# Kernel optimization log

Measured on AMD Instinct MI355X. Metric: run time of the kernel, lower is better.

## Reference

```python
import jax, jax.numpy as jnp
import numpy as np

IN_DIM = 300
MEM_DIM = 1024
DEPTH = 14  # perfect binary tree in heap order: N = 2**DEPTH - 1 = 16383 nodes


def _init_linear(key, out_dim, in_dim):
    # torch nn.Linear default init: U(-1/sqrt(in), 1/sqrt(in)) for W and b
    s = 1.0 / np.sqrt(in_dim)
    kw, kb = jax.random.split(key)
    W = jax.random.uniform(kw, (out_dim, in_dim), jnp.float32, -s, s)
    b = jax.random.uniform(kb, (out_dim,), jnp.float32, -s, s)
    return W, b


def setup_inputs() -> dict:
    key = jax.random.key(0)
    keys = jax.random.split(key, 9)
    N = 2 ** DEPTH - 1
    inp = {"embs": jax.random.normal(keys[0], (N, IN_DIM), jnp.float32)}
    gates = [("ix", IN_DIM), ("ih", MEM_DIM), ("fx", IN_DIM), ("fh", MEM_DIM),
             ("ox", IN_DIM), ("oh", MEM_DIM), ("ux", IN_DIM), ("uh", MEM_DIM)]
    for k, (name, d) in zip(keys[1:], gates):
        W, b = _init_linear(k, MEM_DIM, d)
        inp["W" + name] = W
        inp["b" + name] = b
    inp["depth"] = DEPTH
    return inp


def _lin(x, W, b):
    return x @ W.T + b


def reference(embs, Wix, bix, Wih, bih, Wfx, bfx, Wfh, bfh,
              Wox, box, Woh, boh, Wux, bux, Wuh, buh, depth):
    # Child-Sum TreeLSTM on a perfect binary tree (heap order), processed
    # bottom-up, batching all nodes of a level into single GEMMs.
    h = c = None
    for lvl in range(depth - 1, -1, -1):
        n = 2 ** lvl
        x = embs[n - 1:2 * n - 1]  # [n, in_dim], nodes of this level
        if h is None:
            # leaves: original code feeds a single zero child -> h_sum = 0
            # and f * child_c = 0 regardless of f
            hsum = jnp.zeros((n, MEM_DIM), embs.dtype)
            fc = jnp.zeros((n, MEM_DIM), embs.dtype)
        else:
            hc = h.reshape(n, 2, MEM_DIM)  # children hidden states
            cc = c.reshape(n, 2, MEM_DIM)  # children cell states
            hsum = hc.sum(axis=1)
            # per-child forget gate: sigmoid(fh(h_k) + fx(x))
            f = jax.nn.sigmoid(jnp.einsum('nkd,md->nkm', hc, Wfh) + bfh
                               + _lin(x, Wfx, bfx)[:, None, :])
            fc = (f * cc).sum(axis=1)
        i = jax.nn.sigmoid(_lin(x, Wix, bix) + _lin(hsum, Wih, bih))
        o = jax.nn.sigmoid(_lin(x, Wox, box) + _lin(hsum, Woh, boh))
        u = jnp.tanh(_lin(x, Wux, bux) + _lin(hsum, Wuh, buh))
        c = i * u + fc
        h = o * jnp.tanh(c)
    return jnp.stack([c[0], h[0]])  # root state (c, h): [2, MEM_DIM]
```

## Files before the change

kernel.cpp:

```cpp
#include <hip/hip_runtime.h>
#include <hip/hip_bf16.h>

#define IN_DIM 300
#define XDIM   320
#define MEM    1024
#define NTREE  16383

typedef _Float16 half8 __attribute__((ext_vector_type(8)));
typedef float    f32x4 __attribute__((ext_vector_type(4)));

__device__ __forceinline__ float sigf(float x) { return 1.0f / (1.0f + __expf(-x)); }
__device__ __forceinline__ float tanhfast(float x) { return 2.0f / (1.0f + __expf(-2.0f * x)) - 1.0f; }

#define GLOAD_LDS16(g, l) \
    __builtin_amdgcn_global_load_lds((const __attribute__((address_space(1))) void*)(g), \
                                     (__attribute__((address_space(3))) void*)(l), 16, 0, 0)

__global__ void pack_kernel(
    const float* __restrict__ embs,
    const float* __restrict__ Wix, const float* __restrict__ bix,
    const float* __restrict__ Wih, const float* __restrict__ bih,
    const float* __restrict__ Wfx, const float* __restrict__ bfx,
    const float* __restrict__ Wfh, const float* __restrict__ bfh,
    const float* __restrict__ Wox, const float* __restrict__ box_,
    const float* __restrict__ Woh, const float* __restrict__ boh,
    const float* __restrict__ Wux, const float* __restrict__ bux,
    const float* __restrict__ Wuh, const float* __restrict__ buh,
    _Float16* __restrict__ Wiou16, _Float16* __restrict__ Wfh16,
    _Float16* __restrict__ x16, _Float16* __restrict__ Bx)
{
    long long idx = (long long)blockIdx.x * blockDim.x + threadIdx.x;
    const long long n_wiou = 3072LL * 1024;
    const long long n_wfh  = 1024LL * 1024;
    const long long n_x    = 16384LL * XDIM;
    const long long n_bx   = 4096LL * XDIM;
    if (idx < n_wiou) {
        int m = (int)(idx >> 10), k = (int)(idx & 1023);
        int g = m >> 10, mm = m & 1023;
        const float* W = (g == 0) ? Wih : (g == 1) ? Woh : Wuh;
        Wiou16[idx] = (_Float16)W[(long long)mm * MEM + k];
        return;
    }
    idx -= n_wiou;
    if (idx < n_wfh) {
        Wfh16[idx] = (_Float16)Wfh[idx];
        return;
    }
    idx -= n_wfh;
    if (idx < n_x) {
        int node = (int)(idx / XDIM), j = (int)(idx % XDIM);
        float v = 0.f;
        if (node < NTREE) {
            if (j < IN_DIM) v = embs[(long long)node * IN_DIM + j];
            else if (j == IN_DIM) v = 1.0f;
        }
        x16[idx] = (_Float16)v;
        return;
    }
    idx -= n_x;
    if (idx < n_bx) {
        int r = (int)(idx / XDIM), j = (int)(idx % XDIM);
        int g = r >> 10, mm = r & 1023;
        const float* Wx = (g == 0) ? Wix : (g == 1) ? Wox : (g == 2) ? Wux : Wfx;
        const float* b1 = (g == 0) ? bix : (g == 1) ? box_ : (g == 2) ? bux : bfx;
        const float* b2 = (g == 0) ? bih : (g == 1) ? boh : (g == 2) ? buh : bfh;
        float v = 0.f;
        if (j < IN_DIM) v = Wx[(long long)mm * IN_DIM + j];
        else if (j == IN_DIM) v = b1[mm] + b2[mm];
        Bx[idx] = (_Float16)v;
    }
}

template<int BM, int BN, int BK>
__device__ __forceinline__ void gemm_tile(
    const _Float16* __restrict__ A, int lda,
    const _Float16* __restrict__ B, int ldb,
    _Float16* __restrict__ C, int ldc, int K,
    _Float16* ldsA, _Float16* ldsB)
{
    constexpr int FM = BM / 32, FN = BN / 32;
    constexpr int CPR = BK / 8, SWM = CPR - 1;
    constexpr int ACH = BM * BK / 2048, BCH = BN * BK / 2048;

    int tid = threadIdx.x, wave = tid >> 6, lane = tid & 63;
    int wr = (wave >> 1) * (BM / 2), wc = (wave & 1) * (BN / 2);
    int kq = (lane >> 4) * 8, rs = lane & 15;
    f32x4 acc[FM][FN] = {};

    for (int k0 = 0; k0 < K; k0 += BK) {
#pragma unroll
        for (int j = 0; j < ACH; ++j) {
            int c = j * 256 + tid;
            int row = c / CPR;
            int s = (c ^ row) & SWM;
            GLOAD_LDS16(A + (long long)row * lda + k0 + s * 8,
                        &ldsA[(j * 256 + wave * 64) * 8]);
        }
#pragma unroll
        for (int j = 0; j < BCH; ++j) {
            int c = j * 256 + tid;
            int row = c / CPR;
            int s = (c ^ row) & SWM;
            GLOAD_LDS16(B + (long long)row * ldb + k0 + s * 8,
                        &ldsB[(j * 256 + wave * 64) * 8]);
        }
        __syncthreads();
#pragma unroll
        for (int kk = 0; kk < BK; kk += 32) {
            half8 a[FM], b[FN];
#pragma unroll
            for (int i = 0; i < FM; ++i) {
                int r = wr + i * 16 + rs;
                int s = ((kk + kq) >> 3) ^ (r & SWM);
                a[i] = *(const half8*)&ldsA[r * BK + s * 8];
            }
#pragma unroll
            for (int i = 0; i < FN; ++i) {
                int r = wc + i * 16 + rs;
                int s = ((kk + kq) >> 3) ^ (r & SWM);
                b[i] = *(const half8*)&ldsB[r * BK + s * 8];
            }
#pragma unroll
            for (int mi = 0; mi < FM; ++mi)
#pragma unroll
                for (int ni = 0; ni < FN; ++ni)
                    acc[mi][ni] = __builtin_amdgcn_mfma_f32_16x16x32_f16(a[mi], b[ni], acc[mi][ni], 0, 0, 0);
        }
        __syncthreads();
    }
    int crb = wr + (lane >> 4) * 4, ccb = wc + rs;
#pragma unroll
    for (int mi = 0; mi < FM; ++mi)
#pragma unroll
        for (int i = 0; i < 4; ++i) {
            long long r = crb + mi * 16 + i;
#pragma unroll
            for (int ni = 0; ni < FN; ++ni)
                C[r * ldc + ccb + ni * 16] = (_Float16)acc[mi][ni][i];
        }
}

template<int BM, int BN, int BK>
__global__ __launch_bounds__(256) void gemm_f16(
    const _Float16* __restrict__ A, int lda,
    const _Float16* __restrict__ B, int ldb,
    _Float16* __restrict__ C, int ldc, int K)
{
    __shared__ __align__(16) _Float16 ldsA[BM * BK];
    __shared__ __align__(16) _Float16 ldsB[BN * BK];
    gemm_tile<BM, BN, BK>(A + (long long)blockIdx.x * BM * lda, lda,
                          B + (long long)blockIdx.y * BN * ldb, ldb,
                          C + (long long)blockIdx.x * BM * ldc + (long long)blockIdx.y * BN,
                          ldc, K, ldsA, ldsB);
}

template<int BM1, int BM2, int BK>
__global__ __launch_bounds__(256) void gemm_level(
    const _Float16* __restrict__ Hsum, const _Float16* __restrict__ Hc,
    const _Float16* __restrict__ Wiou, const _Float16* __restrict__ Wf,
    _Float16* __restrict__ houpre, _Float16* __restrict__ fpre,
    int G1, int G2)
{
    constexpr int BMX = (BM1 > BM2) ? BM1 : BM2;
    __shared__ __align__(16) _Float16 ldsA[BMX * BK];
    __shared__ __align__(16) _Float16 ldsB[128 * BK];
    int bx = blockIdx.x;
    if (bx < G1 * 24) {
        int nb = bx / G1, mb = bx % G1;
        gemm_tile<BM1, 128, BK>(Hsum + (long long)mb * BM1 * 1024, 1024,
                                Wiou + (long long)nb * 128 * 1024, 1024,
                                houpre + (long long)mb * BM1 * 3072 + nb * 128, 3072,
                                1024, ldsA, ldsB);
    } else {
        int b2 = bx - G1 * 24;
        int nb = b2 / G2, mb = b2 % G2;
        gemm_tile<BM2, 128, BK>(Hc + (long long)mb * BM2 * 1024, 1024,
                                Wf + (long long)nb * 128 * 1024, 1024,
                                fpre + (long long)mb * BM2 * 1024 + nb * 128, 1024,
                                1024, ldsA, ldsB);
    }
}

__global__ __launch_bounds__(256) void leaf_fused(
    const _Float16* __restrict__ x16, const _Float16* __restrict__ Bx,
    _Float16* __restrict__ cleaf, _Float16* __restrict__ hleaf,
    _Float16* __restrict__ hsum)
{
    constexpr int BK = 32, CPR = 4, SWM = 3;
    __shared__ __align__(16) _Float16 lA[64 * BK];
    __shared__ __align__(16) _Float16 lB[384 * BK];
    int tid = threadIdx.x, wave = tid >> 6, lane = tid & 63;
    int kq = (lane >> 4) * 8, rs = lane & 15;
    int wr = (wave >> 1) * 32, wc = (wave & 1) * 64;
    int m0 = blockIdx.x * 64, c0 = blockIdx.y * 128;
    const _Float16* A = x16 + (size_t)(8191 + m0) * XDIM;

    f32x4 acc[3][2][4] = {};
    for (int t = 0; t < 10; ++t) {
        int k0 = t * BK;
        {
            int c = tid, row = c / CPR, s = (c ^ row) & SWM;
            GLOAD_LDS16(A + (long long)row * XDIM + k0 + s * 8, &lA[(wave * 64) * 8]);
        }
#pragma unroll
        for (int j = 0; j < 6; ++j) {
            int c = j * 256 + tid;
            int row = c / CPR, s = (c ^ row) & SWM;
            int g = row >> 7, rr = row & 127;
            GLOAD_LDS16(Bx + (long long)(g * 1024 + c0 + rr) * XDIM + k0 + s * 8,
                        &lB[(j * 256 + wave * 64) * 8]);
        }
        __syncthreads();
        half8 a[2], b[3][4];
#pragma unroll
        for (int mi = 0; mi < 2; ++mi) {
            int r = wr + mi * 16 + rs;
            int s = (kq >> 3) ^ (r & SWM);
            a[mi] = *(const half8*)&lA[r * BK + s * 8];
        }
#pragma unroll
        for (int g = 0; g < 3; ++g)
#pragma unroll
            for (int nj = 0; nj < 4; ++nj) {
                int r = g * 128 + wc + nj * 16 + rs;
                int s = (kq >> 3) ^ (r & SWM);
                b[g][nj] = *(const half8*)&lB[r * BK + s * 8];
            }
#pragma unroll
        for (int g = 0; g < 3; ++g)
#pragma unroll
            for (int mi = 0; mi < 2; ++mi)
#pragma unroll
                for (int nj = 0; nj < 4; ++nj)
                    acc[g][mi][nj] = __builtin_amdgcn_mfma_f32_16x16x32_f16(a[mi], b[g][nj], acc[g][mi][nj], 0, 0, 0);
        __syncthreads();
    }
    int lrb = wr + (lane >> 4) * 4;
#pragma unroll
    for (int mi = 0; mi < 2; ++mi)
#pragma unroll
        for (int nj = 0; nj < 4; ++nj) {
            int col = c0 + wc + nj * 16 + rs;
            float hpair = 0.f;
#pragma unroll
            for (int i = 0; i < 4; ++i) {
                long long l = m0 + lrb + mi * 16 + i;
                float cc = sigf(acc[0][mi][nj][i]) * tanhfast(acc[2][mi][nj][i]);
                float hh = sigf(acc[1][mi][nj][i]) * tanhfast(cc);
                cleaf[l * 1024 + col] = (_Float16)cc;
                hleaf[l * 1024 + col] = (_Float16)hh;
                if (i & 1) hsum[(l >> 1) * 1024 + col] = (_Float16)(hpair + hh);
                else hpair = hh;
            }
        }
}

template<bool C16>
__global__ void combine_level(
    const _Float16* __restrict__ houpre, const _Float16* __restrict__ fpre,
    const void* __restrict__ cprevp,
    const _Float16* __restrict__ Xp,
    float* __restrict__ cout, _Float16* __restrict__ hout, _Float16* __restrict__ hsum,
    int n, int gx0, float* __restrict__ fin)
{
    int idx = blockIdx.x * blockDim.x + threadIdx.x;
    int npairs = (n > 1) ? (n >> 1) : 1;
    if (idx >= npairs * 128) return;
    int r = idx >> 7, m8 = (idx & 127) * 8;
    float hs[8];
#pragma unroll
    for (int j = 0; j < 8; ++j) hs[j] = 0.f;
    int pmax = (n > 1) ? 2 : 1;
    for (int t = 0; t < pmax; ++t) {
        int p = 2 * r + t;
        long long node = gx0 + p;
        half8 phi = *(const half8*)&houpre[(long long)p * 3072 + m8];
        half8 pho = *(const half8*)&houpre[(long long)p * 3072 + 1024 + m8];
        half8 phu = *(const half8*)&houpre[(long long)p * 3072 + 2048 + m8];
        half8 pxi = *(const half8*)&Xp[node * 4096 + m8];
        half8 pxo = *(const half8*)&Xp[node * 4096 + 1024 + m8];
        half8 pxu = *(const half8*)&Xp[node * 4096 + 2048 + m8];
        half8 pxf = *(const half8*)&Xp[node * 4096 + 3072 + m8];
        half8 pf0 = *(const half8*)&fpre[(long long)(2 * p) * 1024 + m8];
        half8 pf1 = *(const half8*)&fpre[(long long)(2 * p + 1) * 1024 + m8];
        float c0[8], c1[8];
        if (C16) {
            const _Float16* cp = (const _Float16*)cprevp;
            half8 a = *(const half8*)&cp[(long long)(2 * p) * 1024 + m8];
            half8 b = *(const half8*)&cp[(long long)(2 * p + 1) * 1024 + m8];
#pragma unroll
            for (int j = 0; j < 8; ++j) { c0[j] = (float)a[j]; c1[j] = (float)b[j]; }
        } else {
            const float* cp = (const float*)cprevp;
            f32x4 a0 = *(const f32x4*)&cp[(long long)(2 * p) * 1024 + m8];
            f32x4 a1 = *(const f32x4*)&cp[(long long)(2 * p) * 1024 + m8 + 4];
            f32x4 b0 = *(const f32x4*)&cp[(long long)(2 * p + 1) * 1024 + m8];
            f32x4 b1 = *(const f32x4*)&cp[(long long)(2 * p + 1) * 1024 + m8 + 4];
#pragma unroll
            for (int j = 0; j < 4; ++j) { c0[j] = a0[j]; c0[j + 4] = a1[j]; c1[j] = b0[j]; c1[j + 4] = b1[j]; }
        }
        float cw[8], hw[8];
#pragma unroll
        for (int j = 0; j < 8; ++j) {
            float i  = sigf((float)phi[j] + (float)pxi[j]);
            float o  = sigf((float)pho[j] + (float)pxo[j]);
            float u  = tanhfast((float)phu[j] + (float)pxu[j]);
            float f0 = sigf((float)pf0[j] + (float)pxf[j]);
            float f1 = sigf((float)pf1[j] + (float)pxf[j]);
            float c = i * u + f0 * c0[j] + f1 * c1[j];
            float h = o * tanhfast(c);
            cw[j] = c; hw[j] = h; hs[j] += h;
        }
        if (fin) {
            f32x4 v0 = {cw[0], cw[1], cw[2], cw[3]}, v1 = {cw[4], cw[5], cw[6], cw[7]};
            f32x4 w0 = {hw[0], hw[1], hw[2], hw[3]}, w1 = {hw[4], hw[5], hw[6], hw[7]};
            *(f32x4*)&fin[m8] = v0;            *(f32x4*)&fin[m8 + 4] = v1;
            *(f32x4*)&fin[1024 + m8] = w0;     *(f32x4*)&fin[1024 + m8 + 4] = w1;
        } else {
            f32x4 v0 = {cw[0], cw[1], cw[2], cw[3]}, v1 = {cw[4], cw[5], cw[6], cw[7]};
            *(f32x4*)&cout[(long long)p * 1024 + m8] = v0;
            *(f32x4*)&cout[(long long)p * 1024 + m8 + 4] = v1;
            half8 hv;
#pragma unroll
            for (int j = 0; j < 8; ++j) hv[j] = (_Float16)hw[j];
            *(half8*)&hout[(long long)p * 1024 + m8] = hv;
        }
    }
    if (!fin) {
        half8 sv;
#pragma unroll
        for (int j = 0; j < 8; ++j) sv[j] = (_Float16)hs[j];
        *(half8*)&hsum[(long long)r * 1024 + m8] = sv;
    }
}

extern "C" void kernel_launch(void* const* d_in, const int* in_sizes, int n_in,
                              void* d_out, int out_size, void* d_ws, size_t ws_size,
                              hipStream_t stream)
{
    const float* embs = (const float*)d_in[0];
    const float* Wix = (const float*)d_in[1];  const float* bix = (const float*)d_in[2];
    const float* Wih = (const float*)d_in[3];  const float* bih = (const float*)d_in[4];
    const float* Wfx = (const float*)d_in[5];  const float* bfx = (const float*)d_in[6];
    const float* Wfh = (const float*)d_in[7];  const float* bfh = (const float*)d_in[8];
    const float* Wox = (const float*)d_in[9];  const float* box_ = (const float*)d_in[10];
    const float* Woh = (const float*)d_in[11]; const float* boh = (const float*)d_in[12];
    const float* Wux = (const float*)d_in[13]; const float* bux = (const float*)d_in[14];
    const float* Wuh = (const float*)d_in[15]; const float* buh = (const float*)d_in[16];

    char* p = (char*)d_ws;
    auto carve = [&](size_t bytes) -> char* {
        char* r = p; p += (bytes + 255) & ~(size_t)255; return r;
    };
    _Float16* Wiou16 = (_Float16*)carve((size_t)3072 * 1024 * 2);
    _Float16* Wfh16  = (_Float16*)carve((size_t)1024 * 1024 * 2);
    _Float16* Xp     = (_Float16*)carve((size_t)8192 * 4096 * 2);
    _Float16* houpre = (_Float16*)carve((size_t)4096 * 3072 * 2);
    _Float16* fpre   = (_Float16*)carve((size_t)8192 * 1024 * 2);
    _Float16* H_A    = (_Float16*)carve((size_t)8192 * 1024 * 2);
    _Float16* H_B    = (_Float16*)carve((size_t)4096 * 1024 * 2);
    _Float16* HsumA  = (_Float16*)carve((size_t)4096 * 1024 * 2);
    _Float16* HsumB  = (_Float16*)carve((size_t)4096 * 1024 * 2);
    _Float16* Cleaf  = (_Float16*)carve((size_t)8192 * 1024 * 2);
    float*    Cping  = (float*)carve((size_t)4096 * 1024 * 4);
    float*    Cpong  = (float*)carve((size_t)2048 * 1024 * 4);
    _Float16* x16 = fpre;
    _Float16* Bx  = fpre + (size_t)16384 * XDIM;

    {
        long long tot = 3072LL * 1024 + 1024LL * 1024 + 16384LL * XDIM + 4096LL * XDIM;
        pack_kernel<<<dim3((int)((tot + 255) / 256)), dim3(256), 0, stream>>>(
            embs, Wix, bix, Wih, bih, Wfx, bfx, Wfh, bfh,
            Wox, box_, Woh, boh, Wux, bux, Wuh, buh,
            Wiou16, Wfh16, x16, Bx);
    }

    gemm_f16<128, 128, 32><<<dim3(64, 32), dim3(256), 0, stream>>>(
        x16, XDIM, Bx, XDIM, Xp, 4096, XDIM);
    leaf_fused<<<dim3(128, 8), dim3(256), 0, stream>>>(x16, Bx, Cleaf, H_A, HsumA);

    const void* cprev = Cleaf;
    float* cbufs[2] = {Cping, Cpong};
    _Float16* hsums[2] = {HsumA, HsumB};
    int ci = 0, si = 0;
    _Float16* hcur = H_A;
    _Float16* hnext = H_B;

    for (int lvl = 12; lvl >= 0; --lvl) {
        int n = 1 << lvl;
        int G1, G2;
        if (n >= 1024) {
            G1 = n / 128; G2 = 2 * n / 128;
            gemm_level<128, 128, 32><<<dim3(G1 * 24 + G2 * 8), dim3(256), 0, stream>>>(
                hsums[si], hcur, Wiou16, Wfh16, houpre, fpre, G1, G2);
        } else if (n >= 128) {
            G1 = n / 128; G2 = 2 * n / 128;
            gemm_level<128, 128, 128><<<dim3(G1 * 24 + G2 * 8), dim3(256), 0, stream>>>(
                hsums[si], hcur, Wiou16, Wfh16, houpre, fpre, G1, G2);
        } else if (n == 64) {
            G1 = 1; G2 = 1;
            gemm_level<64, 128, 128><<<dim3(G1 * 24 + G2 * 8), dim3(256), 0, stream>>>(
                hsums[si], hcur, Wiou16, Wfh16, houpre, fpre, G1, G2);
        } else {
            G1 = 1; G2 = 1;
            gemm_level<64, 64, 128><<<dim3(G1 * 24 + G2 * 8), dim3(256), 0, stream>>>(
                hsums[si], hcur, Wiou16, Wfh16, houpre, fpre, G1, G2);
        }

        int npairs = (n > 1) ? (n >> 1) : 1;
        int blocks = (npairs * 128 + 255) / 256;
        float* fin = (lvl == 0) ? (float*)d_out : nullptr;
        if (lvl == 12)
            combine_level<true><<<dim3(blocks), dim3(256), 0, stream>>>(
                houpre, fpre, cprev, Xp, cbufs[ci], hnext, hsums[si ^ 1], n, n - 1, fin);
        else
            combine_level<false><<<dim3(blocks), dim3(256), 0, stream>>>(
                houpre, fpre, cprev, Xp, cbufs[ci], hnext, hsums[si ^ 1], n, n - 1, fin);

        cprev = cbufs[ci];
        ci ^= 1; si ^= 1;
        _Float16* tmp = hcur; hcur = hnext; hnext = tmp;
    }
}
```

Baseline: 448.8 us.

## Add split-K tail GEMMs, fuse gate activations into GEMM epilogue, merge leaf launches

```diff
diff --git a/kernel.cpp b/kernel.cpp
--- a/kernel.cpp
+++ b/kernel.cpp
@@ -72,11 +72,11 @@
 }
 
 template<int BM, int BN, int BK>
-__device__ __forceinline__ void gemm_tile(
+__device__ __forceinline__ void gemm_core(
     const _Float16* __restrict__ A, int lda,
-    const _Float16* __restrict__ B, int ldb,
-    _Float16* __restrict__ C, int ldc, int K,
-    _Float16* ldsA, _Float16* ldsB)
+    const _Float16* __restrict__ B, int ldb, int K,
+    _Float16* ldsA, _Float16* ldsB,
+    f32x4 (&acc)[BM / 32][BN / 32])
 {
     constexpr int FM = BM / 32, FN = BN / 32;
     constexpr int CPR = BK / 8, SWM = CPR - 1;
@@ -85,7 +85,6 @@
     int tid = threadIdx.x, wave = tid >> 6, lane = tid & 63;
     int wr = (wave >> 1) * (BM / 2), wc = (wave & 1) * (BN / 2);
     int kq = (lane >> 4) * 8, rs = lane & 15;
-    f32x4 acc[FM][FN] = {};
 
     for (int k0 = 0; k0 < K; k0 += BK) {
 #pragma unroll
@@ -128,161 +127,189 @@
         }
         __syncthreads();
     }
-    int crb = wr + (lane >> 4) * 4, ccb = wc + rs;
-#pragma unroll
-    for (int mi = 0; mi < FM; ++mi)
-#pragma unroll
-        for (int i = 0; i < 4; ++i) {
-            long long r = crb + mi * 16 + i;
-#pragma unroll
-            for (int ni = 0; ni < FN; ++ni)
-                C[r * ldc + ccb + ni * 16] = (_Float16)acc[mi][ni][i];
-        }
-}
-
-template<int BM, int BN, int BK>
-__global__ __launch_bounds__(256) void gemm_f16(
-    const _Float16* __restrict__ A, int lda,
-    const _Float16* __restrict__ B, int ldb,
-    _Float16* __restrict__ C, int ldc, int K)
-{
-    __shared__ __align__(16) _Float16 ldsA[BM * BK];
-    __shared__ __align__(16) _Float16 ldsB[BN * BK];
-    gemm_tile<BM, BN, BK>(A + (long long)blockIdx.x * BM * lda, lda,
-                          B + (long long)blockIdx.y * BN * ldb, ldb,
-                          C + (long long)blockIdx.x * BM * ldc + (long long)blockIdx.y * BN,
-                          ldc, K, ldsA, ldsB);
+}
+
+__global__ __launch_bounds__(256) void proj_fused(
+    const _Float16* __restrict__ x16, const _Float16* __restrict__ Bx,
+    _Float16* __restrict__ Xp,
+    _Float16* __restrict__ cleaf, _Float16* __restrict__ hleaf,
+    _Float16* __restrict__ hsum)
+{
+    __shared__ __align__(16) _Float16 lds[448 * 32];
+    int tid = threadIdx.x, wave = tid >> 6, lane = tid & 63;
+    int kq = (lane >> 4) * 8, rs = lane & 15;
+
+    if (blockIdx.x < 2048) {
+        int mb = blockIdx.x & 63, nb = blockIdx.x >> 6;
+        f32x4 acc[4][4] = {};
+        gemm_core<128, 128, 32>(x16 + (long long)mb * 128 * XDIM, XDIM,
+                                Bx + (long long)nb * 128 * XDIM, XDIM, XDIM,
+                                lds, lds + 4096, acc);
+        int wr = (wave >> 1) * 64, wc = (wave & 1) * 64;
+        int crb = wr + (lane >> 4) * 4, ccb = wc + rs;
+#pragma unroll
+        for (int mi = 0; mi < 4; ++mi)
+#pragma unroll
+            for (int i = 0; i < 4; ++i) {
+                long long r = mb * 128 + crb + mi * 16 + i;
+#pragma unroll
+                for (int ni = 0; ni < 4; ++ni)
+                    Xp[r * 4096 + nb * 128 + ccb + ni * 16] = (_Float16)acc[mi][ni][i];
+            }
+        return;
+    }
+    {
+        constexpr int BK = 32, CPR = 4, SWM = 3;
+        _Float16* lA = lds;
+        _Float16* lB = lds + 64 * 32;
+        int bid = (int)blockIdx.x - 2048;
+        int m0 = (bid & 127) * 64, c0 = (bid >> 7) * 128;
+        int wr = (wave >> 1) * 32, wc = (wave & 1) * 64;
+        const _Float16* A = x16 + (size_t)(8191 + m0) * XDIM;
+
+        f32x4 acc[3][2][4] = {};
+        for (int t = 0; t < 10; ++t) {
+            int k0 = t * BK;
+            {
+                int c = tid, row = c / CPR, s = (c ^ row) & SWM;
+                GLOAD_LDS16(A + (long long)row * XDIM + k0 + s * 8, &lA[(wave * 64) * 8]);
+            }
+#pragma unroll
+            for (int j = 0; j < 6; ++j) {
+                int c = j * 256 + tid;
+                int row = c / CPR, s = (c ^ row) & SWM;
+                int g = row >> 7, rr = row & 127;
+                GLOAD_LDS16(Bx + (long long)(g * 1024 + c0 + rr) * XDIM + k0 + s * 8,
+                            &lB[(j * 256 + wave * 64) * 8]);
+            }
+            __syncthreads();
+            half8 a[2], b[3][4];
+#pragma unroll
+            for (int mi = 0; mi < 2; ++mi) {
+                int r = wr + mi * 16 + rs;
+                int s = (kq >> 3) ^ (r & SWM);
+                a[mi] = *(const half8*)&lA[r * BK + s * 8];
+            }
+#pragma unroll
+            for (int g = 0; g < 3; ++g)
+#pragma unroll
+                for (int nj = 0; nj < 4; ++nj) {
+                    int r = g * 128 + wc + nj * 16 + rs;
+                    int s = (kq >> 3) ^ (r & SWM);
+                    b[g][nj] = *(const half8*)&lB[r * BK + s * 8];
+                }
+#pragma unroll
+            for (int g = 0; g < 3; ++g)
+#pragma unroll
+                for (int mi = 0; mi < 2; ++mi)
+#pragma unroll
+                    for (int nj = 0; nj < 4; ++nj)
+                        acc[g][mi][nj] = __builtin_amdgcn_mfma_f32_16x16x32_f16(a[mi], b[g][nj], acc[g][mi][nj], 0, 0, 0);
+            __syncthreads();
+        }
+        int lrb = wr + (lane >> 4) * 4;
+#pragma unroll
+        for (int mi = 0; mi < 2; ++mi)
+#pragma unroll
+            for (int nj = 0; nj < 4; ++nj) {
+                int col = c0 + wc + nj * 16 + rs;
+                float hpair = 0.f;
+#pragma unroll
+                for (int i = 0; i < 4; ++i) {
+                    long long l = m0 + lrb + mi * 16 + i;
+                    float cc = sigf(acc[0][mi][nj][i]) * tanhfast(acc[2][mi][nj][i]);
+                    float hh = sigf(acc[1][mi][nj][i]) * tanhfast(cc);
+                    cleaf[l * 1024 + col] = (_Float16)cc;
+                    hleaf[l * 1024 + col] = (_Float16)hh;
+                    if (i & 1) hsum[(l >> 1) * 1024 + col] = (_Float16)(hpair + hh);
+                    else hpair = hh;
+                }
+            }
+    }
 }
 
 template<int BM1, int BM2, int BK>
-__global__ __launch_bounds__(256) void gemm_level(
+__global__ __launch_bounds__(256) void gemm_level_act(
     const _Float16* __restrict__ Hsum, const _Float16* __restrict__ Hc,
     const _Float16* __restrict__ Wiou, const _Float16* __restrict__ Wf,
-    _Float16* __restrict__ houpre, _Float16* __restrict__ fpre,
-    int G1, int G2)
+    const _Float16* __restrict__ Xp,
+    _Float16* __restrict__ houact, _Float16* __restrict__ fact,
+    int G1, int G2, int n)
 {
     constexpr int BMX = (BM1 > BM2) ? BM1 : BM2;
     __shared__ __align__(16) _Float16 ldsA[BMX * BK];
     __shared__ __align__(16) _Float16 ldsB[128 * BK];
+    int tid = threadIdx.x, wave = tid >> 6, lane = tid & 63;
     int bx = blockIdx.x;
     if (bx < G1 * 24) {
         int nb = bx / G1, mb = bx % G1;
-        gemm_tile<BM1, 128, BK>(Hsum + (long long)mb * BM1 * 1024, 1024,
-                                Wiou + (long long)nb * 128 * 1024, 1024,
-                                houpre + (long long)mb * BM1 * 3072 + nb * 128, 3072,
-                                1024, ldsA, ldsB);
+        f32x4 acc[BM1 / 32][4] = {};
+        gemm_core<BM1, 128, BK>(Hsum + (long long)mb * BM1 * 1024, 1024,
+                                Wiou + (long long)nb * 128 * 1024, 1024, 1024,
+                                ldsA, ldsB, acc);
+        int gate = nb >> 3;
+        int wr = (wave >> 1) * (BM1 / 2), wc = (wave & 1) * 64;
+        int crb = wr + (lane >> 4) * 4, ccb = wc + (lane & 15);
+#pragma unroll
+        for (int mi = 0; mi < BM1 / 32; ++mi)
+#pragma unroll
+            for (int i = 0; i < 4; ++i) {
+                long long row = mb * BM1 + crb + mi * 16 + i;
+                long long node = (n - 1) + row;
+#pragma unroll
+                for (int ni = 0; ni < 4; ++ni) {
+                    int col = nb * 128 + ccb + ni * 16;
+                    float v = acc[mi][ni][i] + (float)Xp[node * 4096 + col];
+                    float a = (gate == 2) ? tanhfast(v) : sigf(v);
+                    houact[row * 3072 + col] = (_Float16)a;
+                }
+            }
     } else {
         int b2 = bx - G1 * 24;
         int nb = b2 / G2, mb = b2 % G2;
-        gemm_tile<BM2, 128, BK>(Hc + (long long)mb * BM2 * 1024, 1024,
-                                Wf + (long long)nb * 128 * 1024, 1024,
-                                fpre + (long long)mb * BM2 * 1024 + nb * 128, 1024,
-                                1024, ldsA, ldsB);
-    }
-}
-
-__global__ __launch_bounds__(256) void leaf_fused(
-    const _Float16* __restrict__ x16, const _Float16* __restrict__ Bx,
-    _Float16* __restrict__ cleaf, _Float16* __restrict__ hleaf,
-    _Float16* __restrict__ hsum)
-{
-    constexpr int BK = 32, CPR = 4, SWM = 3;
-    __shared__ __align__(16) _Float16 lA[64 * BK];
-    __shared__ __align__(16) _Float16 lB[384 * BK];
-    int tid = threadIdx.x, wave = tid >> 6, lane = tid & 63;
-    int kq = (lane >> 4) * 8, rs = lane & 15;
-    int wr = (wave >> 1) * 32, wc = (wave & 1) * 64;
-    int m0 = blockIdx.x * 64, c0 = blockIdx.y * 128;
-    const _Float16* A = x16 + (size_t)(8191 + m0) * XDIM;
-
-    f32x4 acc[3][2][4] = {};
-    for (int t = 0; t < 10; ++t) {
-        int k0 = t * BK;
-        {
-            int c = tid, row = c / CPR, s = (c ^ row) & SWM;
-            GLOAD_LDS16(A + (long long)row * XDIM + k0 + s * 8, &lA[(wave * 64) * 8]);
-        }
-#pragma unroll
-        for (int j = 0; j < 6; ++j) {
-            int c = j * 256 + tid;
-            int row = c / CPR, s = (c ^ row) & SWM;
-            int g = row >> 7, rr = row & 127;
-            GLOAD_LDS16(Bx + (long long)(g * 1024 + c0 + rr) * XDIM + k0 + s * 8,
-                        &lB[(j * 256 + wave * 64) * 8]);
-        }
-        __syncthreads();
-        half8 a[2], b[3][4];
-#pragma unroll
-        for (int mi = 0; mi < 2; ++mi) {
-            int r = wr + mi * 16 + rs;
-            int s = (kq >> 3) ^ (r & SWM);
-            a[mi] = *(const half8*)&lA[r * BK + s * 8];
-        }
-#pragma unroll
-        for (int g = 0; g < 3; ++g)
-#pragma unroll
-            for (int nj = 0; nj < 4; ++nj) {
-                int r = g * 128 + wc + nj * 16 + rs;
-                int s = (kq >> 3) ^ (r & SWM);
-                b[g][nj] = *(const half8*)&lB[r * BK + s * 8];
-            }
-#pragma unroll
-        for (int g = 0; g < 3; ++g)
-#pragma unroll
-            for (int mi = 0; mi < 2; ++mi)
-#pragma unroll
-                for (int nj = 0; nj < 4; ++nj)
-                    acc[g][mi][nj] = __builtin_amdgcn_mfma_f32_16x16x32_f16(a[mi], b[g][nj], acc[g][mi][nj], 0, 0, 0);
-        __syncthreads();
-    }
-    int lrb = wr + (lane >> 4) * 4;
-#pragma unroll
-    for (int mi = 0; mi < 2; ++mi)
-#pragma unroll
-        for (int nj = 0; nj < 4; ++nj) {
-            int col = c0 + wc + nj * 16 + rs;
-            float hpair = 0.f;
+        f32x4 acc[BM2 / 32][4] = {};
+        gemm_core<BM2, 128, BK>(Hc + (long long)mb * BM2 * 1024, 1024,
+                                Wf + (long long)nb * 128 * 1024, 1024, 1024,
+                                ldsA, ldsB, acc);
+        int wr = (wave >> 1) * (BM2 / 2), wc = (wave & 1) * 64;
+        int crb = wr + (lane >> 4) * 4, ccb = wc + (lane & 15);
+#pragma unroll
+        for (int mi = 0; mi < BM2 / 32; ++mi)
 #pragma unroll
             for (int i = 0; i < 4; ++i) {
-                long long l = m0 + lrb + mi * 16 + i;
-                float cc = sigf(acc[0][mi][nj][i]) * tanhfast(acc[2][mi][nj][i]);
-                float hh = sigf(acc[1][mi][nj][i]) * tanhfast(cc);
-                cleaf[l * 1024 + col] = (_Float16)cc;
-                hleaf[l * 1024 + col] = (_Float16)hh;
-                if (i & 1) hsum[(l >> 1) * 1024 + col] = (_Float16)(hpair + hh);
-                else hpair = hh;
-            }
-        }
+                long long row = mb * BM2 + crb + mi * 16 + i;
+                long long node = (n - 1) + (row >> 1);
+#pragma unroll
+                for (int ni = 0; ni < 4; ++ni) {
+                    int col = nb * 128 + ccb + ni * 16;
+                    float v = acc[mi][ni][i] + (float)Xp[node * 4096 + 3072 + col];
+                    fact[row * 1024 + col] = (_Float16)sigf(v);
+                }
+            }
+    }
 }
 
 template<bool C16>
-__global__ void combine_level(
-    const _Float16* __restrict__ houpre, const _Float16* __restrict__ fpre,
+__global__ void combine_act(
+    const _Float16* __restrict__ houact, const _Float16* __restrict__ fact,
     const void* __restrict__ cprevp,
-    const _Float16* __restrict__ Xp,
     float* __restrict__ cout, _Float16* __restrict__ hout, _Float16* __restrict__ hsum,
-    int n, int gx0, float* __restrict__ fin)
+    int n)
 {
     int idx = blockIdx.x * blockDim.x + threadIdx.x;
-    int npairs = (n > 1) ? (n >> 1) : 1;
+    int npairs = n >> 1;
     if (idx >= npairs * 128) return;
     int r = idx >> 7, m8 = (idx & 127) * 8;
     float hs[8];
 #pragma unroll
     for (int j = 0; j < 8; ++j) hs[j] = 0.f;
-    int pmax = (n > 1) ? 2 : 1;
-    for (int t = 0; t < pmax; ++t) {
+    for (int t = 0; t < 2; ++t) {
         int p = 2 * r + t;
-        long long node = gx0 + p;
-        half8 phi = *(const half8*)&houpre[(long long)p * 3072 + m8];
-        half8 pho = *(const half8*)&houpre[(long long)p * 3072 + 1024 + m8];
-        half8 phu = *(const half8*)&houpre[(long long)p * 3072 + 2048 + m8];
-        half8 pxi = *(const half8*)&Xp[node * 4096 + m8];
-        half8 pxo = *(const half8*)&Xp[node * 4096 + 1024 + m8];
-        half8 pxu = *(const half8*)&Xp[node * 4096 + 2048 + m8];
-        half8 pxf = *(const half8*)&Xp[node * 4096 + 3072 + m8];
-        half8 pf0 = *(const half8*)&fpre[(long long)(2 * p) * 1024 + m8];
-        half8 pf1 = *(const half8*)&fpre[(long long)(2 * p + 1) * 1024 + m8];
+        half8 vi = *(const half8*)&houact[(long long)p * 3072 + m8];
+        half8 vo = *(const half8*)&houact[(long long)p * 3072 + 1024 + m8];
+        half8 vu = *(const half8*)&houact[(long long)p * 3072 + 2048 + m8];
+        half8 f0 = *(const half8*)&fact[(long long)(2 * p) * 1024 + m8];
+        half8 f1 = *(const half8*)&fact[(long long)(2 * p + 1) * 1024 + m8];
         float c0[8], c1[8];
         if (C16) {
             const _Float16* cp = (const _Float16*)cprevp;
@@ -302,12 +329,128 @@
         float cw[8], hw[8];
 #pragma unroll
         for (int j = 0; j < 8; ++j) {
-            float i  = sigf((float)phi[j] + (float)pxi[j]);
-            float o  = sigf((float)pho[j] + (float)pxo[j]);
-            float u  = tanhfast((float)phu[j] + (float)pxu[j]);
-            float f0 = sigf((float)pf0[j] + (float)pxf[j]);
-            float f1 = sigf((float)pf1[j] + (float)pxf[j]);
-            float c = i * u + f0 * c0[j] + f1 * c1[j];
+            float c = (float)vi[j] * (float)vu[j]
+                    + (float)f0[j] * c0[j] + (float)f1[j] * c1[j];
+            float h = (float)vo[j] * tanhfast(c);
+            cw[j] = c; hw[j] = h; hs[j] += h;
+        }
+        f32x4 v0 = {cw[0], cw[1], cw[2], cw[3]}, v1 = {cw[4], cw[5], cw[6], cw[7]};
+        *(f32x4*)&cout[(long long)p * 1024 + m8] = v0;
+        *(f32x4*)&cout[(long long)p * 1024 + m8 + 4] = v1;
+        half8 hv;
+#pragma unroll
+        for (int j = 0; j < 8; ++j) hv[j] = (_Float16)hw[j];
+        *(half8*)&hout[(long long)p * 1024 + m8] = hv;
+    }
+    half8 sv;
+#pragma unroll
+    for (int j = 0; j < 8; ++j) sv[j] = (_Float16)hs[j];
+    *(half8*)&hsum[(long long)r * 1024 + m8] = sv;
+}
+
+__global__ __launch_bounds__(256) void tail_sk(
+    const _Float16* __restrict__ Hs, const _Float16* __restrict__ Hc,
+    const _Float16* __restrict__ Wiou, const _Float16* __restrict__ Wf,
+    float* __restrict__ houp, float* __restrict__ fp,
+    int n, int PTn, int PT2n)
+{
+    __shared__ __align__(16) _Float16 ldsA[64 * 128];
+    __shared__ __align__(16) _Float16 ldsB[128 * 128];
+    int tid = threadIdx.x, wave = tid >> 6, lane = tid & 63;
+    int T = PTn * 24 + PT2n * 8;
+    int s = blockIdx.x / T, r = blockIdx.x % T;
+    int k0 = s * 256;
+    f32x4 acc[2][4] = {};
+    int wr = (wave >> 1) * 32, wc = (wave & 1) * 64;
+    int crb = wr + (lane >> 4) * 4, ccb = wc + (lane & 15);
+    if (r < PTn * 24) {
+        int nb = r / PTn, mb = r % PTn;
+        gemm_core<64, 128, 128>(Hs + (long long)mb * 64 * 1024 + k0, 1024,
+                                Wiou + (long long)nb * 128 * 1024 + k0, 1024, 256,
+                                ldsA, ldsB, acc);
+#pragma unroll
+        for (int mi = 0; mi < 2; ++mi)
+#pragma unroll
+            for (int i = 0; i < 4; ++i) {
+                int row = mb * 64 + crb + mi * 16 + i;
+                if (row >= n) continue;
+#pragma unroll
+                for (int ni = 0; ni < 4; ++ni)
+                    houp[((long long)s * n + row) * 3072 + nb * 128 + ccb + ni * 16] = acc[mi][ni][i];
+            }
+    } else {
+        int b2 = r - PTn * 24;
+        int nb = b2 / PT2n, mb = b2 % PT2n;
+        gemm_core<64, 128, 128>(Hc + (long long)mb * 64 * 1024 + k0, 1024,
+                                Wf + (long long)nb * 128 * 1024 + k0, 1024, 256,
+                                ldsA, ldsB, acc);
+#pragma unroll
+        for (int mi = 0; mi < 2; ++mi)
+#pragma unroll
+            for (int i = 0; i < 4; ++i) {
+                int row = mb * 64 + crb + mi * 16 + i;
+                if (row >= 2 * n) continue;
+#pragma unroll
+                for (int ni = 0; ni < 4; ++ni)
+                    fp[((long long)s * 2 * n + row) * 1024 + nb * 128 + ccb + ni * 16] = acc[mi][ni][i];
+            }
+    }
+}
+
+__global__ void combine_tail(
+    const float* __restrict__ houp, const float* __restrict__ fp,
+    const float* __restrict__ cprev, const _Float16* __restrict__ Xp,
+    float* __restrict__ cout, _Float16* __restrict__ hout, _Float16* __restrict__ hsum,
+    int n, float* __restrict__ fin)
+{
+    int idx = blockIdx.x * blockDim.x + threadIdx.x;
+    int npairs = (n > 1) ? (n >> 1) : 1;
+    if (idx >= npairs * 128) return;
+    int r = idx >> 7, m8 = (idx & 127) * 8;
+    float hs[8];
+#pragma unroll
+    for (int j = 0; j < 8; ++j) hs[j] = 0.f;
+    int pmax = (n > 1) ? 2 : 1;
+    for (int t = 0; t < pmax; ++t) {
+        int p = 2 * r + t;
+        long long node = (n - 1) + p;
+        float gi[8], go[8], gu[8], q0[8], q1[8];
+        half8 xi = *(const half8*)&Xp[node * 4096 + m8];
+        half8 xo = *(const half8*)&Xp[node * 4096 + 1024 + m8];
+        half8 xu = *(const half8*)&Xp[node * 4096 + 2048 + m8];
+        half8 xf = *(const half8*)&Xp[node * 4096 + 3072 + m8];
+#pragma unroll
+        for (int j = 0; j < 8; ++j) {
+            gi[j] = (float)xi[j]; go[j] = (float)xo[j]; gu[j] = (float)xu[j];
+            q0[j] = (float)xf[j]; q1[j] = (float)xf[j];
+        }
+#pragma unroll
+        for (int s = 0; s < 4; ++s) {
+            const float* hb = houp + ((long long)s * n + p) * 3072;
+#pragma unroll
+            for (int j = 0; j < 8; ++j) {
+                gi[j] += hb[m8 + j];
+                go[j] += hb[1024 + m8 + j];
+                gu[j] += hb[2048 + m8 + j];
+            }
+            const float* fb0 = fp + ((long long)s * 2 * n + 2 * p) * 1024;
+            const float* fb1 = fp + ((long long)s * 2 * n + 2 * p + 1) * 1024;
+#pragma unroll
+            for (int j = 0; j < 8; ++j) {
+                q0[j] += fb0[m8 + j];
+                q1[j] += fb1[m8 + j];
+            }
+        }
+        float cw[8], hw[8];
+#pragma unroll
+        for (int j = 0; j < 8; ++j) {
+            float i  = sigf(gi[j]);
+            float o  = sigf(go[j]);
+            float u  = tanhfast(gu[j]);
+            float f0 = sigf(q0[j]);
+            float f1 = sigf(q1[j]);
+            float c = i * u + f0 * cprev[(long long)(2 * p) * 1024 + m8 + j]
+                            + f1 * cprev[(long long)(2 * p + 1) * 1024 + m8 + j];
             float h = o * tanhfast(c);
             cw[j] = c; hw[j] = h; hs[j] += h;
         }
@@ -355,8 +498,8 @@
     _Float16* Wiou16 = (_Float16*)carve((size_t)3072 * 1024 * 2);
     _Float16* Wfh16  = (_Float16*)carve((size_t)1024 * 1024 * 2);
     _Float16* Xp     = (_Float16*)carve((size_t)8192 * 4096 * 2);
-    _Float16* houpre = (_Float16*)carve((size_t)4096 * 3072 * 2);
-    _Float16* fpre   = (_Float16*)carve((size_t)8192 * 1024 * 2);
+    _Float16* houact = (_Float16*)carve((size_t)4096 * 3072 * 2);
+    _Float16* fact   = (_Float16*)carve((size_t)8192 * 1024 * 2);
     _Float16* H_A    = (_Float16*)carve((size_t)8192 * 1024 * 2);
     _Float16* H_B    = (_Float16*)carve((size_t)4096 * 1024 * 2);
     _Float16* HsumA  = (_Float16*)carve((size_t)4096 * 1024 * 2);
@@ -364,8 +507,10 @@
     _Float16* Cleaf  = (_Float16*)carve((size_t)8192 * 1024 * 2);
     float*    Cping  = (float*)carve((size_t)4096 * 1024 * 4);
     float*    Cpong  = (float*)carve((size_t)2048 * 1024 * 4);
-    _Float16* x16 = fpre;
-    _Float16* Bx  = fpre + (size_t)16384 * XDIM;
+    float*    houp4  = (float*)carve((size_t)4 * 256 * 3072 * 4);
+    float*    fp4    = (float*)carve((size_t)4 * 512 * 1024 * 4);
+    _Float16* x16 = fact;
+    _Float16* Bx  = fact + (size_t)16384 * XDIM;
 
     {
         long long tot = 3072LL * 1024 + 1024LL * 1024 + 16384LL * XDIM + 4096LL * XDIM;
@@ -375,9 +520,8 @@
             Wiou16, Wfh16, x16, Bx);
     }
 
-    gemm_f16<128, 128, 32><<<dim3(64, 32), dim3(256), 0, stream>>>(
-        x16, XDIM, Bx, XDIM, Xp, 4096, XDIM);
-    leaf_fused<<<dim3(128, 8), dim3(256), 0, stream>>>(x16, Bx, Cleaf, H_A, HsumA);
+    proj_fused<<<dim3(3072), dim3(256), 0, stream>>>(
+        x16, Bx, Xp, Cleaf, H_A, HsumA);
 
     const void* cprev = Cleaf;
     float* cbufs[2] = {Cping, Cpong};
@@ -386,39 +530,41 @@
     _Float16* hcur = H_A;
     _Float16* hnext = H_B;
 
-    for (int lvl = 12; lvl >= 0; --lvl) {
+    for (int lvl = 12; lvl >= 9; --lvl) {
         int n = 1 << lvl;
-        int G1, G2;
-        if (n >= 1024) {
-            G1 = n / 128; G2 = 2 * n / 128;
-            gemm_level<128, 128, 32><<<dim3(G1 * 24 + G2 * 8), dim3(256), 0, stream>>>(
-                hsums[si], hcur, Wiou16, Wfh16, houpre, fpre, G1, G2);
-        } else if (n >= 128) {
-            G1 = n / 128; G2 = 2 * n / 128;
-            gemm_level<128, 128, 128><<<dim3(G1 * 24 + G2 * 8), dim3(256), 0, stream>>>(
-                hsums[si], hcur, Wiou16, Wfh16, houpre, fpre, G1, G2);
-        } else if (n == 64) {
-            G1 = 1; G2 = 1;
-            gemm_level<64, 128, 128><<<dim3(G1 * 24 + G2 * 8), dim3(256), 0, stream>>>(
-                hsums[si], hcur, Wiou16, Wfh16, houpre, fpre, G1, G2);
-        } else {
-            G1 = 1; G2 = 1;
-            gemm_level<64, 64, 128><<<dim3(G1 * 24 + G2 * 8), dim3(256), 0, stream>>>(
-                hsums[si], hcur, Wiou16, Wfh16, houpre, fpre, G1, G2);
-        }
-
-        int npairs = (n > 1) ? (n >> 1) : 1;
-        int blocks = (npairs * 128 + 255) / 256;
-        float* fin = (lvl == 0) ? (float*)d_out : nullptr;
+        int G1 = n / 128, G2 = 2 * n / 128;
+        if (n >= 1024)
+            gemm_level_act<128, 128, 32><<<dim3(G1 * 24 + G2 * 8), dim3(256), 0, stream>>>(
+                hsums[si], hcur, Wiou16, Wfh16, Xp, houact, fact, G1, G2, n);
+        else
+            gemm_level_act<128, 128, 128><<<dim3(G1 * 24 + G2 * 8), dim3(256), 0, stream>>>(
+                hsums[si], hcur, Wiou16, Wfh16, Xp, houact, fact, G1, G2, n);
+        int blocks = ((n >> 1) * 128 + 255) / 256;
         if (lvl == 12)
-            combine_level<true><<<dim3(blocks), dim3(256), 0, stream>>>(
-                houpre, fpre, cprev, Xp, cbufs[ci], hnext, hsums[si ^ 1], n, n - 1, fin);
+            combine_act<true><<<dim3(blocks), dim3(256), 0, stream>>>(
+                houact, fact, cprev, cbufs[ci], hnext, hsums[si ^ 1], n);
         else
-            combine_level<false><<<dim3(blocks), dim3(256), 0, stream>>>(
-                houpre, fpre, cprev, Xp, cbufs[ci], hnext, hsums[si ^ 1], n, n - 1, fin);
-
+            combine_act<false><<<dim3(blocks), dim3(256), 0, stream>>>(
+                houact, fact, cprev, cbufs[ci], hnext, hsums[si ^ 1], n);
         cprev = cbufs[ci];
         ci ^= 1; si ^= 1;
         _Float16* tmp = hcur; hcur = hnext; hnext = tmp;
     }
-}
+
+    for (int lvl = 8; lvl >= 0; --lvl) {
+        int n = 1 << lvl;
+        int PTn = (n + 63) / 64, PT2n = (2 * n + 63) / 64;
+        int T = PTn * 24 + PT2n * 8;
+        tail_sk<<<dim3(T * 4), dim3(256), 0, stream>>>(
+            hsums[si], hcur, Wiou16, Wfh16, houp4, fp4, n, PTn, PT2n);
+        int npairs = (n > 1) ? (n >> 1) : 1;
+        int blocks = (npairs * 128 + 255) / 256;
+        combine_tail<<<dim3(blocks), dim3(256), 0, stream>>>(
+            houp4, fp4, (const float*)cprev, Xp,
+            cbufs[ci], hnext, hsums[si ^ 1], n,
+            (lvl == 0) ? (float*)d_out : nullptr);
+        cprev = cbufs[ci];
+        ci ^= 1; si ^= 1;
+        _Float16* tmp = hcur; hcur = hnext; hnext = tmp;
+    }
+}
```

Measured after the change: 474.2 us. +5.7%, slower.
